# Performance work log

Measured on AMD Instinct MI355X. Metric: run time of the kernel, lower is better.

## Reference

```python
import jax, jax.numpy as jnp
import numpy as np

DIM = 1024
NUM_EXPERTS = 8
ACTIVE_EXPERTS = 2
EXPERT_DIM = 2048


def setup_inputs() -> dict:
    key = jax.random.key(0)
    k1, k2, k3, k4 = jax.random.split(key, 4)
    x = jax.random.normal(k1, (1, 2048, DIM), dtype=jnp.float32)
    gate_w = jax.random.normal(k2, (NUM_EXPERTS, DIM), dtype=jnp.float32) * 0.02
    balance_bias = jnp.zeros((NUM_EXPERTS,), dtype=jnp.float32)
    w1 = jax.random.normal(k3, (NUM_EXPERTS, EXPERT_DIM, DIM), dtype=jnp.float32) * 0.02
    w2 = jax.random.normal(k4, (NUM_EXPERTS, DIM, EXPERT_DIM), dtype=jnp.float32) * 0.02
    return {"x": x, "gate_w": gate_w, "balance_bias": balance_bias, "w1": w1, "w2": w2}


def reference(x, gate_w, balance_bias, w1, w2):
    B, S, D = x.shape
    T = B * S
    xf = x.reshape(T, D)
    # gating: sigmoid scores with load-balance bias, then top-k
    gate_logits = jnp.einsum('td,ed->te', xf, gate_w)
    gate_scores = jax.nn.sigmoid(gate_logits + balance_bias)
    topk_scores, topk_idx = jax.lax.top_k(gate_scores, ACTIVE_EXPERTS)
    topk_scores = topk_scores / (topk_scores.sum(axis=-1, keepdims=True) + 1e-6)
    # scatter normalized scores into dense combine weights [T, E]
    comb = jnp.zeros((T, NUM_EXPERTS), dtype=x.dtype)
    comb = comb.at[jnp.arange(T)[:, None], topk_idx].add(topk_scores)
    # expert FFNs (dense over experts; combine weight zeroes unselected)
    h = jax.nn.silu(jnp.einsum('td,ehd->teh', xf, w1))   # [T, E, expert_dim]
    expert_out = jnp.einsum('teh,edh->ted', h, w2)        # [T, E, D]
    out = jnp.einsum('te,ted->td', comb, expert_out)
    return out.reshape(B, S, D)
```

## Files before the change

### kernel.cpp

```cpp
#include <hip/hip_runtime.h>

#define T 2048
#define DIM 1024
#define NE 8
#define ED 2048
#define NSLOT (T * 2)
#define KSPLIT 2

#define BM 128
#define BN 64
#define BK 32

typedef __attribute__((ext_vector_type(8))) short s8v;
typedef __attribute__((ext_vector_type(4))) float f32x4;

__device__ __forceinline__ short f2bf(float f) {
    union { float f; unsigned u; } v;
    v.f = f;
    unsigned r = 0x7FFFu + ((v.u >> 16) & 1u);
    v.u += r;
    return (short)(v.u >> 16);
}

__device__ __forceinline__ float bf2f(short s) {
    union { unsigned u; float f; } v;
    v.u = ((unsigned)(unsigned short)s) << 16;
    return v.f;
}

__device__ __forceinline__ unsigned pkbf2(float lo, float hi) {
    union { float f; unsigned u; } a, b;
    a.f = lo; b.f = hi;
    return __builtin_amdgcn_perm(b.u + 0x8000u, a.u + 0x8000u, 0x07060302u);
}

__device__ __forceinline__ void glds16(const void* g, void* l) {
    __builtin_amdgcn_global_load_lds(
        (const __attribute__((address_space(1))) void*)g,
        (__attribute__((address_space(3))) void*)l, 16, 0, 0);
}

__global__ __launch_bounds__(256) void convert_kernel(const float* __restrict__ src,
                                                      short* __restrict__ dst, int n8) {
    int stride = gridDim.x * 256;
    for (int i = blockIdx.x * 256 + threadIdx.x; i < n8; i += stride) {
        float4 a = ((const float4*)src)[2 * i];
        float4 b = ((const float4*)src)[2 * i + 1];
        uint4 o = { pkbf2(a.x, a.y), pkbf2(a.z, a.w), pkbf2(b.x, b.y), pkbf2(b.z, b.w) };
        ((uint4*)dst)[i] = o;
    }
}

__global__ void router_kernel(const float* __restrict__ x,
                              const float* __restrict__ gw,
                              const float* __restrict__ bias,
                              short* __restrict__ xb,
                              int* __restrict__ counts,
                              int* __restrict__ top2i,
                              float* __restrict__ top2w) {
    int wid = threadIdx.x >> 6;
    int lane = threadIdx.x & 63;
    int t = blockIdx.x * 4 + wid;

    const float* xr = x + (size_t)t * DIM + lane * 16;
    float4 xv[4];
#pragma unroll
    for (int j = 0; j < 4; ++j) xv[j] = *(const float4*)(xr + j * 4);

    s8v o0, o1;
#pragma unroll
    for (int j = 0; j < 2; ++j) {
        o0[j * 4 + 0] = f2bf(xv[j].x); o0[j * 4 + 1] = f2bf(xv[j].y);
        o0[j * 4 + 2] = f2bf(xv[j].z); o0[j * 4 + 3] = f2bf(xv[j].w);
        o1[j * 4 + 0] = f2bf(xv[j + 2].x); o1[j * 4 + 1] = f2bf(xv[j + 2].y);
        o1[j * 4 + 2] = f2bf(xv[j + 2].z); o1[j * 4 + 3] = f2bf(xv[j + 2].w);
    }
    *(s8v*)(xb + (size_t)t * DIM + lane * 16) = o0;
    *(s8v*)(xb + (size_t)t * DIM + lane * 16 + 8) = o1;

    float sc[NE];
#pragma unroll
    for (int e = 0; e < NE; ++e) {
        const float* gr = gw + e * DIM + lane * 16;
        float p = 0.f;
#pragma unroll
        for (int j = 0; j < 4; ++j) {
            float4 g = *(const float4*)(gr + j * 4);
            p += xv[j].x * g.x + xv[j].y * g.y + xv[j].z * g.z + xv[j].w * g.w;
        }
#pragma unroll
        for (int off = 32; off; off >>= 1) p += __shfl_xor(p, off, 64);
        sc[e] = 1.f / (1.f + __expf(-(p + bias[e])));
    }
    int b0 = 0; float s0 = sc[0];
#pragma unroll
    for (int e = 1; e < NE; ++e) if (sc[e] > s0) { s0 = sc[e]; b0 = e; }
    int b1 = -1; float s1 = -1e30f;
#pragma unroll
    for (int e = 0; e < NE; ++e) if (e != b0 && sc[e] > s1) { s1 = sc[e]; b1 = e; }
    float inv = 1.f / (s0 + s1 + 1e-6f);
    if (lane == 0) {
        top2i[t * 2 + 0] = b0; top2i[t * 2 + 1] = b1;
        top2w[t * 2 + 0] = s0 * inv; top2w[t * 2 + 1] = s1 * inv;
        atomicAdd(&counts[b0], 1);
        atomicAdd(&counts[b1], 1);
    }
}

__global__ __launch_bounds__(256) void plan_kernel(
    const int* __restrict__ counts, const int* __restrict__ top2i,
    int* __restrict__ offsets, int* __restrict__ tok_list, int* __restrict__ slot_of) {
    __shared__ int soff[NE];
    __shared__ int srun[NE];
    if (threadIdx.x == 0) {
        int a = 0;
        for (int e = 0; e < NE; ++e) { soff[e] = a; offsets[e] = a; a += counts[e]; srun[e] = 0; }
    }
    __syncthreads();
    for (int t = threadIdx.x; t < T; t += 256) {
#pragma unroll
        for (int k = 0; k < 2; ++k) {
            int e = top2i[t * 2 + k];
            int pos = atomicAdd(&srun[e], 1);
            int slot = soff[e] + pos;
            tok_list[slot] = t;
            slot_of[t * 2 + k] = slot;
        }
    }
}

template <int BF>
__global__ __launch_bounds__(256) void ffn1_kernel(
    const short* __restrict__ xb, const float* __restrict__ w1,
    const short* __restrict__ wb,
    const int* __restrict__ counts, const int* __restrict__ offsets,
    const int* __restrict__ tok_list, short* __restrict__ h) {
    int e = blockIdx.x & 7;
    int j = blockIdx.x >> 3;
    int cnt = counts[e];
    const int NT = ED / BN;
    int mt = (cnt + BM - 1) / BM;
    if (j >= mt * NT) return;
    int m0 = (j / NT) * BM;
    int n0 = (j % NT) * BN;
    int off = offsets[e];

    __shared__ __align__(16) short As[2][4][BM][8];
    __shared__ __align__(16) short Bs[2][4][BN][8];

    int tid = threadIdx.x;
    int lane = tid & 63, w = tid >> 6;
    int mo = w * 32;
    int lrow = lane & 15, lq = lane >> 4;

    f32x4 acc[2][4];
#pragma unroll
    for (int mi = 0; mi < 2; ++mi)
#pragma unroll
        for (int ni = 0; ni < 4; ++ni) acc[mi][ni] = (f32x4){0.f, 0.f, 0.f, 0.f};

    int ra0 = m0 + lane;      if (ra0 > cnt - 1) ra0 = cnt - 1;
    int ra1 = m0 + 64 + lane; if (ra1 > cnt - 1) ra1 = cnt - 1;
    const short* a0 = xb + (size_t)tok_list[off + ra0] * DIM + w * 8;
    const short* a1 = xb + (size_t)tok_list[off + ra1] * DIM + w * 8;

    const short* b0 = wb + ((size_t)e * ED + n0 + lane) * DIM + w * 8;
    int br = tid >> 2, bq = tid & 3;
    const float* bp = w1 + ((size_t)e * ED + n0 + br) * DIM + bq * 8;

    const int NK = DIM / BK;

    if constexpr (BF) {
        auto stage = [&](int s, int b) {
            int k0 = s * BK;
            glds16(a0 + k0, &As[b][w][0][0]);
            glds16(a1 + k0, &As[b][w][64][0]);
            glds16(b0 + k0, &Bs[b][w][0][0]);
        };
        stage(0, 0);
        for (int kk = 0; kk < NK; ++kk) {
            int cur = kk & 1, nxt = cur ^ 1;
            __syncthreads();
            if (kk + 1 < NK) stage(kk + 1, nxt);
            s8v af[2], bfr[4];
#pragma unroll
            for (int mi = 0; mi < 2; ++mi) af[mi] = *(const s8v*)&As[cur][lq][mo + mi * 16 + lrow][0];
#pragma unroll
            for (int ni = 0; ni < 4; ++ni) bfr[ni] = *(const s8v*)&Bs[cur][lq][ni * 16 + lrow][0];
#pragma unroll
            for (int mi = 0; mi < 2; ++mi)
#pragma unroll
                for (int ni = 0; ni < 4; ++ni)
                    acc[mi][ni] = __builtin_amdgcn_mfma_f32_16x16x32_bf16(af[mi], bfr[ni], acc[mi][ni], 0, 0, 0);
        }
    } else {
        float4 L0, L1;
        glds16(a0, &As[0][w][0][0]);
        glds16(a1, &As[0][w][64][0]);
        L0 = *(const float4*)(bp); L1 = *(const float4*)(bp + 4);
        {
            uint4 p0 = { pkbf2(L0.x, L0.y), pkbf2(L0.z, L0.w), pkbf2(L1.x, L1.y), pkbf2(L1.z, L1.w) };
            *(uint4*)&Bs[0][bq][br][0] = p0;
        }
        L0 = *(const float4*)(bp + BK); L1 = *(const float4*)(bp + BK + 4);
        for (int kk = 0; kk < NK; ++kk) {
            int cur = kk & 1, nxt = cur ^ 1;
            __syncthreads();
            if (kk + 1 < NK) {
                int k0 = (kk + 1) * BK;
                glds16(a0 + k0, &As[nxt][w][0][0]);
                glds16(a1 + k0, &As[nxt][w][64][0]);
                uint4 p0 = { pkbf2(L0.x, L0.y), pkbf2(L0.z, L0.w), pkbf2(L1.x, L1.y), pkbf2(L1.z, L1.w) };
                *(uint4*)&Bs[nxt][bq][br][0] = p0;
                if (kk + 2 < NK) {
                    const float* bpp = bp + (kk + 2) * BK;
                    L0 = *(const float4*)(bpp); L1 = *(const float4*)(bpp + 4);
                }
            }
            s8v af[2], bfr[4];
#pragma unroll
            for (int mi = 0; mi < 2; ++mi) af[mi] = *(const s8v*)&As[cur][lq][mo + mi * 16 + lrow][0];
#pragma unroll
            for (int ni = 0; ni < 4; ++ni) bfr[ni] = *(const s8v*)&Bs[cur][lq][ni * 16 + lrow][0];
#pragma unroll
            for (int mi = 0; mi < 2; ++mi)
#pragma unroll
                for (int ni = 0; ni < 4; ++ni)
                    acc[mi][ni] = __builtin_amdgcn_mfma_f32_16x16x32_bf16(af[mi], bfr[ni], acc[mi][ni], 0, 0, 0);
        }
    }

#pragma unroll
    for (int mi = 0; mi < 2; ++mi) {
#pragma unroll
        for (int ni = 0; ni < 4; ++ni) {
            int ln = n0 + ni * 16 + lrow;
#pragma unroll
            for (int r = 0; r < 4; ++r) {
                int row = m0 + mo + mi * 16 + lq * 4 + r;
                if (row < cnt) {
                    float v = acc[mi][ni][r];
                    v = v / (1.f + __expf(-v));
                    h[(size_t)(off + row) * ED + ln] = f2bf(v);
                }
            }
        }
    }
}

template <int BF>
__global__ __launch_bounds__(256) void ffn2_kernel(
    const short* __restrict__ h, const float* __restrict__ w2,
    const short* __restrict__ wb,
    const int* __restrict__ counts, const int* __restrict__ offsets,
    short* __restrict__ eo) {
    int e = blockIdx.x & 7;
    int j = blockIdx.x >> 3;
    int cnt = counts[e];
    const int NT = DIM / BN;
    int mt = (cnt + BM - 1) / BM;
    if (j >= mt * NT * KSPLIT) return;
    int ksp = j & 1; j >>= 1;
    int m0 = (j / NT) * BM;
    int n0 = (j % NT) * BN;
    int off = offsets[e];
    const int kbase = ksp * (ED / KSPLIT);

    __shared__ __align__(16) short As[2][4][BM][8];
    __shared__ __align__(16) short Bs[2][4][BN][8];

    int tid = threadIdx.x;
    int lane = tid & 63, w = tid >> 6;
    int mo = w * 32;
    int lrow = lane & 15, lq = lane >> 4;

    f32x4 acc[2][4];
#pragma unroll
    for (int mi = 0; mi < 2; ++mi)
#pragma unroll
        for (int ni = 0; ni < 4; ++ni) acc[mi][ni] = (f32x4){0.f, 0.f, 0.f, 0.f};

    int ra0 = m0 + lane;      if (ra0 > cnt - 1) ra0 = cnt - 1;
    int ra1 = m0 + 64 + lane; if (ra1 > cnt - 1) ra1 = cnt - 1;
    const short* a0 = h + (size_t)(off + ra0) * ED + kbase + w * 8;
    const short* a1 = h + (size_t)(off + ra1) * ED + kbase + w * 8;

    const short* b0 = wb + ((size_t)e * DIM + n0 + lane) * ED + kbase + w * 8;
    int br = tid >> 2, bq = tid & 3;
    const float* bp = w2 + ((size_t)e * DIM + n0 + br) * ED + kbase + bq * 8;

    const int NK = (ED / KSPLIT) / BK;

    if constexpr (BF) {
        auto stage = [&](int s, int b) {
            int k0 = s * BK;
            glds16(a0 + k0, &As[b][w][0][0]);
            glds16(a1 + k0, &As[b][w][64][0]);
            glds16(b0 + k0, &Bs[b][w][0][0]);
        };
        stage(0, 0);
        for (int kk = 0; kk < NK; ++kk) {
            int cur = kk & 1, nxt = cur ^ 1;
            __syncthreads();
            if (kk + 1 < NK) stage(kk + 1, nxt);
            s8v af[2], bfr[4];
#pragma unroll
            for (int mi = 0; mi < 2; ++mi) af[mi] = *(const s8v*)&As[cur][lq][mo + mi * 16 + lrow][0];
#pragma unroll
            for (int ni = 0; ni < 4; ++ni) bfr[ni] = *(const s8v*)&Bs[cur][lq][ni * 16 + lrow][0];
#pragma unroll
            for (int mi = 0; mi < 2; ++mi)
#pragma unroll
                for (int ni = 0; ni < 4; ++ni)
                    acc[mi][ni] = __builtin_amdgcn_mfma_f32_16x16x32_bf16(af[mi], bfr[ni], acc[mi][ni], 0, 0, 0);
        }
    } else {
        float4 L0, L1;
        glds16(a0, &As[0][w][0][0]);
        glds16(a1, &As[0][w][64][0]);
        L0 = *(const float4*)(bp); L1 = *(const float4*)(bp + 4);
        {
            uint4 p0 = { pkbf2(L0.x, L0.y), pkbf2(L0.z, L0.w), pkbf2(L1.x, L1.y), pkbf2(L1.z, L1.w) };
            *(uint4*)&Bs[0][bq][br][0] = p0;
        }
        L0 = *(const float4*)(bp + BK); L1 = *(const float4*)(bp + BK + 4);
        for (int kk = 0; kk < NK; ++kk) {
            int cur = kk & 1, nxt = cur ^ 1;
            __syncthreads();
            if (kk + 1 < NK) {
                int k0 = (kk + 1) * BK;
                glds16(a0 + k0, &As[nxt][w][0][0]);
                glds16(a1 + k0, &As[nxt][w][64][0]);
                uint4 p0 = { pkbf2(L0.x, L0.y), pkbf2(L0.z, L0.w), pkbf2(L1.x, L1.y), pkbf2(L1.z, L1.w) };
                *(uint4*)&Bs[nxt][bq][br][0] = p0;
                if (kk + 2 < NK) {
                    const float* bpp = bp + (kk + 2) * BK;
                    L0 = *(const float4*)(bpp); L1 = *(const float4*)(bpp + 4);
                }
            }
            s8v af[2], bfr[4];
#pragma unroll
            for (int mi = 0; mi < 2; ++mi) af[mi] = *(const s8v*)&As[cur][lq][mo + mi * 16 + lrow][0];
#pragma unroll
            for (int ni = 0; ni < 4; ++ni) bfr[ni] = *(const s8v*)&Bs[cur][lq][ni * 16 + lrow][0];
#pragma unroll
            for (int mi = 0; mi < 2; ++mi)
#pragma unroll
                for (int ni = 0; ni < 4; ++ni)
                    acc[mi][ni] = __builtin_amdgcn_mfma_f32_16x16x32_bf16(af[mi], bfr[ni], acc[mi][ni], 0, 0, 0);
        }
    }

    short* eop = eo + (size_t)ksp * NSLOT * DIM;
#pragma unroll
    for (int mi = 0; mi < 2; ++mi) {
#pragma unroll
        for (int ni = 0; ni < 4; ++ni) {
            int ln = n0 + ni * 16 + lrow;
#pragma unroll
            for (int r = 0; r < 4; ++r) {
                int row = m0 + mo + mi * 16 + lq * 4 + r;
                if (row < cnt) {
                    eop[(size_t)(off + row) * DIM + ln] = f2bf(acc[mi][ni][r]);
                }
            }
        }
    }
}

__global__ __launch_bounds__(256) void combine_kernel(
    const short* __restrict__ eo, const int* __restrict__ slot_of,
    const float* __restrict__ top2w, float* __restrict__ out) {
    int idx = blockIdx.x * 256 + threadIdx.x;
    int t = idx >> 7;
    int c = idx & 127;
    int s0 = slot_of[2 * t], s1 = slot_of[2 * t + 1];
    float w0 = top2w[2 * t], w1 = top2w[2 * t + 1];
    const short* e0 = eo;
    const short* e1 = eo + (size_t)NSLOT * DIM;
    s8v a0 = *(const s8v*)(e0 + (size_t)s0 * DIM + c * 8);
    s8v a1 = *(const s8v*)(e1 + (size_t)s0 * DIM + c * 8);
    s8v b0 = *(const s8v*)(e0 + (size_t)s1 * DIM + c * 8);
    s8v b1 = *(const s8v*)(e1 + (size_t)s1 * DIM + c * 8);
    float4 o[2];
#pragma unroll
    for (int j = 0; j < 8; ++j) {
        float v = w0 * (bf2f(a0[j]) + bf2f(a1[j])) + w1 * (bf2f(b0[j]) + bf2f(b1[j]));
        ((float*)o)[j] = v;
    }
    float4* op = (float4*)(out + (size_t)t * DIM + c * 8);
    op[0] = o[0];
    op[1] = o[1];
}

extern "C" void kernel_launch(void* const* d_in, const int* in_sizes, int n_in,
                              void* d_out, int out_size, void* d_ws, size_t ws_size,
                              hipStream_t stream) {
    const float* x    = (const float*)d_in[0];
    const float* gw   = (const float*)d_in[1];
    const float* bias = (const float*)d_in[2];
    const float* w1   = (const float*)d_in[3];
    const float* w2   = (const float*)d_in[4];
    float* out = (float*)d_out;

    char* ws = (char*)d_ws;
    short* xb = (short*)ws;
    short* h  = (short*)(ws + (4ull << 20));
    short* eo = (short*)(ws + (20ull << 20));
    char* meta = ws + (36ull << 20);
    int*   counts   = (int*)(meta);
    int*   offsets  = (int*)(meta + 64);
    int*   tok_list = (int*)(meta + 128);
    int*   slot_of  = (int*)(meta + 128 + 4 * NSLOT);
    int*   top2i    = (int*)(meta + 128 + 8 * NSLOT);
    float* top2w    = (float*)(meta + 128 + 8 * NSLOT + 8 * T);
    short* wb       = (short*)(ws + (37ull << 20));

    bool bf = ws_size >= (70ull << 20);

    hipMemsetAsync(counts, 0, 32, stream);

    const int GRID_FFN1 = 8 * 16 * (ED / BN);
    const int GRID_FFN2 = 8 * 16 * (DIM / BN) * KSPLIT;

    if (bf) {
        convert_kernel<<<2048, 256, 0, stream>>>(w1, wb, NE * ED * DIM / 8);
    }
    router_kernel<<<T / 4, 256, 0, stream>>>(x, gw, bias, xb, counts, top2i, top2w);
    plan_kernel<<<1, 256, 0, stream>>>(counts, top2i, offsets, tok_list, slot_of);
    if (bf) {
        ffn1_kernel<1><<<GRID_FFN1, 256, 0, stream>>>(xb, w1, wb, counts, offsets, tok_list, h);
        convert_kernel<<<2048, 256, 0, stream>>>(w2, wb, NE * DIM * ED / 8);
        ffn2_kernel<1><<<GRID_FFN2, 256, 0, stream>>>(h, w2, wb, counts, offsets, eo);
    } else {
        ffn1_kernel<0><<<GRID_FFN1, 256, 0, stream>>>(xb, w1, nullptr, counts, offsets, tok_list, h);
        ffn2_kernel<0><<<GRID_FFN2, 256, 0, stream>>>(h, w2, nullptr, counts, offsets, eo);
    }
    combine_kernel<<<T * DIM / 8 / 256, 256, 0, stream>>>(eo, slot_of, top2w, out);
}
```

Before: 347.4 us.

## Pre-tile weights and gathered activations into MFMA-ready layout, drop split-K

```diff
diff --git a/kernel.cpp b/kernel.cpp
--- a/kernel.cpp
+++ b/kernel.cpp
@@ -4,8 +4,8 @@
 #define DIM 1024
 #define NE 8
 #define ED 2048
-#define NSLOT (T * 2)
-#define KSPLIT 2
+#define PSLOT 5120
+#define MT_MAX 16
 
 #define BM 128
 #define BN 64
@@ -40,21 +40,39 @@
         (__attribute__((address_space(3))) void*)l, 16, 0, 0);
 }
 
-__global__ __launch_bounds__(256) void convert_kernel(const float* __restrict__ src,
-                                                      short* __restrict__ dst, int n8) {
-    int stride = gridDim.x * 256;
-    for (int i = blockIdx.x * 256 + threadIdx.x; i < n8; i += stride) {
-        float4 a = ((const float4*)src)[2 * i];
-        float4 b = ((const float4*)src)[2 * i + 1];
-        uint4 o = { pkbf2(a.x, a.y), pkbf2(a.z, a.w), pkbf2(b.x, b.y), pkbf2(b.z, b.w) };
-        ((uint4*)dst)[i] = o;
+__global__ __launch_bounds__(256) void convert1_kernel(const float* __restrict__ w1,
+                                                       short* __restrict__ wbt) {
+    int wid = blockIdx.x * 4 + (threadIdx.x >> 6);
+    int lane = threadIdx.x & 63;
+    int e = wid >> 10, rem = wid & 1023, nb = rem >> 5, kk = rem & 31;
+    const float4* src = (const float4*)(w1 + ((size_t)(e * ED + nb * 64 + lane)) * DIM + kk * 32);
+    short* dst = wbt + ((size_t)(e * 32 + nb) * 128 + kk * 4) * 512 + lane * 8;
+#pragma unroll
+    for (int q = 0; q < 4; ++q) {
+        float4 f0 = src[2 * q], f1 = src[2 * q + 1];
+        uint4 o = { pkbf2(f0.x, f0.y), pkbf2(f0.z, f0.w), pkbf2(f1.x, f1.y), pkbf2(f1.z, f1.w) };
+        *(uint4*)(dst + q * 512) = o;
+    }
+}
+
+__global__ __launch_bounds__(256) void convert2_kernel(const float* __restrict__ w2,
+                                                       short* __restrict__ wbt) {
+    int wid = blockIdx.x * 4 + (threadIdx.x >> 6);
+    int lane = threadIdx.x & 63;
+    int e = wid >> 10, rem = wid & 1023, nb = rem >> 6, kk = rem & 63;
+    const float4* src = (const float4*)(w2 + ((size_t)(e * DIM + nb * 64 + lane)) * ED + kk * 32);
+    short* dst = wbt + ((size_t)(e * 16 + nb) * 256 + kk * 4) * 512 + lane * 8;
+#pragma unroll
+    for (int q = 0; q < 4; ++q) {
+        float4 f0 = src[2 * q], f1 = src[2 * q + 1];
+        uint4 o = { pkbf2(f0.x, f0.y), pkbf2(f0.z, f0.w), pkbf2(f1.x, f1.y), pkbf2(f1.z, f1.w) };
+        *(uint4*)(dst + q * 512) = o;
     }
 }
 
 __global__ void router_kernel(const float* __restrict__ x,
                               const float* __restrict__ gw,
                               const float* __restrict__ bias,
-                              short* __restrict__ xb,
                               int* __restrict__ counts,
                               int* __restrict__ top2i,
                               float* __restrict__ top2w) {
@@ -66,17 +84,6 @@
     float4 xv[4];
 #pragma unroll
     for (int j = 0; j < 4; ++j) xv[j] = *(const float4*)(xr + j * 4);
-
-    s8v o0, o1;
-#pragma unroll
-    for (int j = 0; j < 2; ++j) {
-        o0[j * 4 + 0] = f2bf(xv[j].x); o0[j * 4 + 1] = f2bf(xv[j].y);
-        o0[j * 4 + 2] = f2bf(xv[j].z); o0[j * 4 + 3] = f2bf(xv[j].w);
-        o1[j * 4 + 0] = f2bf(xv[j + 2].x); o1[j * 4 + 1] = f2bf(xv[j + 2].y);
-        o1[j * 4 + 2] = f2bf(xv[j + 2].z); o1[j * 4 + 3] = f2bf(xv[j + 2].w);
-    }
-    *(s8v*)(xb + (size_t)t * DIM + lane * 16) = o0;
-    *(s8v*)(xb + (size_t)t * DIM + lane * 16 + 8) = o1;
 
     float sc[NE];
 #pragma unroll
@@ -109,12 +116,16 @@
 
 __global__ __launch_bounds__(256) void plan_kernel(
     const int* __restrict__ counts, const int* __restrict__ top2i,
-    int* __restrict__ offsets, int* __restrict__ tok_list, int* __restrict__ slot_of) {
+    int* __restrict__ poff, int* __restrict__ tok_list, int* __restrict__ slot_of) {
     __shared__ int soff[NE];
     __shared__ int srun[NE];
     if (threadIdx.x == 0) {
         int a = 0;
-        for (int e = 0; e < NE; ++e) { soff[e] = a; offsets[e] = a; a += counts[e]; srun[e] = 0; }
+        for (int e = 0; e < NE; ++e) {
+            soff[e] = a; poff[e] = a;
+            a += ((counts[e] + 127) >> 7) << 7;
+            srun[e] = 0;
+        }
     }
     __syncthreads();
     for (int t = threadIdx.x; t < T; t += 256) {
@@ -127,23 +138,51 @@
             slot_of[t * 2 + k] = slot;
         }
     }
-}
-
-template <int BF>
+    __syncthreads();
+    for (int e = 0; e < NE; ++e) {
+        int cnt = counts[e];
+        int lim = ((cnt + 127) >> 7) << 7;
+        for (int i = cnt + threadIdx.x; i < lim; i += 256) tok_list[soff[e] + i] = 0;
+    }
+}
+
+__global__ __launch_bounds__(256) void gather_kernel(
+    const float* __restrict__ x, const int* __restrict__ counts,
+    const int* __restrict__ poff, const int* __restrict__ tok_list,
+    short* __restrict__ xgt) {
+    int e = blockIdx.x, mb = blockIdx.y;
+    int cnt = counts[e];
+    int mt = (cnt + 127) >> 7;
+    if (mb >= mt) return;
+    int pb = (poff[e] >> 7) + mb;
+    int r = threadIdx.x & 127, hh = threadIdx.x >> 7;
+    int tok = tok_list[poff[e] + mb * 128 + r];
+    const float4* src = (const float4*)(x + (size_t)tok * DIM + hh * 16);
+    short* dst = xgt + ((size_t)pb * 128 + hh * 2) * 1024 + r * 8;
+#pragma unroll 4
+    for (int kk = 0; kk < DIM / 32; ++kk) {
+        float4 f0 = src[0], f1 = src[1], f2 = src[2], f3 = src[3];
+        uint4 o0 = { pkbf2(f0.x, f0.y), pkbf2(f0.z, f0.w), pkbf2(f1.x, f1.y), pkbf2(f1.z, f1.w) };
+        uint4 o1 = { pkbf2(f2.x, f2.y), pkbf2(f2.z, f2.w), pkbf2(f3.x, f3.y), pkbf2(f3.z, f3.w) };
+        *(uint4*)(dst) = o0;
+        *(uint4*)(dst + 1024) = o1;
+        src += 8;
+        dst += 4 * 1024;
+    }
+}
+
 __global__ __launch_bounds__(256) void ffn1_kernel(
-    const short* __restrict__ xb, const float* __restrict__ w1,
-    const short* __restrict__ wb,
-    const int* __restrict__ counts, const int* __restrict__ offsets,
-    const int* __restrict__ tok_list, short* __restrict__ h) {
+    const short* __restrict__ xgt, const short* __restrict__ wbt,
+    const int* __restrict__ counts, const int* __restrict__ poff,
+    short* __restrict__ ht) {
     int e = blockIdx.x & 7;
     int j = blockIdx.x >> 3;
     int cnt = counts[e];
+    int mt = (cnt + 127) >> 7;
     const int NT = ED / BN;
-    int mt = (cnt + BM - 1) / BM;
     if (j >= mt * NT) return;
-    int m0 = (j / NT) * BM;
-    int n0 = (j % NT) * BN;
-    int off = offsets[e];
+    int mb = j / NT, nb = j % NT;
+    int pb = (poff[e] >> 7) + mb;
 
     __shared__ __align__(16) short As[2][4][BM][8];
     __shared__ __align__(16) short Bs[2][4][BN][8];
@@ -159,112 +198,65 @@
 #pragma unroll
         for (int ni = 0; ni < 4; ++ni) acc[mi][ni] = (f32x4){0.f, 0.f, 0.f, 0.f};
 
-    int ra0 = m0 + lane;      if (ra0 > cnt - 1) ra0 = cnt - 1;
-    int ra1 = m0 + 64 + lane; if (ra1 > cnt - 1) ra1 = cnt - 1;
-    const short* a0 = xb + (size_t)tok_list[off + ra0] * DIM + w * 8;
-    const short* a1 = xb + (size_t)tok_list[off + ra1] * DIM + w * 8;
-
-    const short* b0 = wb + ((size_t)e * ED + n0 + lane) * DIM + w * 8;
-    int br = tid >> 2, bq = tid & 3;
-    const float* bp = w1 + ((size_t)e * ED + n0 + br) * DIM + bq * 8;
-
+    const short* asrc = xgt + (size_t)pb * 128 * 1024;
+    const short* bsrc = wbt + (size_t)(e * 32 + nb) * 128 * 512;
+
+    auto stage = [&](int s, int b) {
+        int p = s * 4 + w;
+        glds16(asrc + (size_t)p * 1024 + lane * 8,       &As[b][w][0][0]);
+        glds16(asrc + (size_t)p * 1024 + 512 + lane * 8, &As[b][w][64][0]);
+        glds16(bsrc + (size_t)p * 512 + lane * 8,        &Bs[b][w][0][0]);
+    };
     const int NK = DIM / BK;
-
-    if constexpr (BF) {
-        auto stage = [&](int s, int b) {
-            int k0 = s * BK;
-            glds16(a0 + k0, &As[b][w][0][0]);
-            glds16(a1 + k0, &As[b][w][64][0]);
-            glds16(b0 + k0, &Bs[b][w][0][0]);
-        };
-        stage(0, 0);
-        for (int kk = 0; kk < NK; ++kk) {
-            int cur = kk & 1, nxt = cur ^ 1;
-            __syncthreads();
-            if (kk + 1 < NK) stage(kk + 1, nxt);
-            s8v af[2], bfr[4];
-#pragma unroll
-            for (int mi = 0; mi < 2; ++mi) af[mi] = *(const s8v*)&As[cur][lq][mo + mi * 16 + lrow][0];
-#pragma unroll
-            for (int ni = 0; ni < 4; ++ni) bfr[ni] = *(const s8v*)&Bs[cur][lq][ni * 16 + lrow][0];
-#pragma unroll
-            for (int mi = 0; mi < 2; ++mi)
-#pragma unroll
-                for (int ni = 0; ni < 4; ++ni)
-                    acc[mi][ni] = __builtin_amdgcn_mfma_f32_16x16x32_bf16(af[mi], bfr[ni], acc[mi][ni], 0, 0, 0);
-        }
-    } else {
-        float4 L0, L1;
-        glds16(a0, &As[0][w][0][0]);
-        glds16(a1, &As[0][w][64][0]);
-        L0 = *(const float4*)(bp); L1 = *(const float4*)(bp + 4);
-        {
-            uint4 p0 = { pkbf2(L0.x, L0.y), pkbf2(L0.z, L0.w), pkbf2(L1.x, L1.y), pkbf2(L1.z, L1.w) };
-            *(uint4*)&Bs[0][bq][br][0] = p0;
-        }
-        L0 = *(const float4*)(bp + BK); L1 = *(const float4*)(bp + BK + 4);
-        for (int kk = 0; kk < NK; ++kk) {
-            int cur = kk & 1, nxt = cur ^ 1;
-            __syncthreads();
-            if (kk + 1 < NK) {
-                int k0 = (kk + 1) * BK;
-                glds16(a0 + k0, &As[nxt][w][0][0]);
-                glds16(a1 + k0, &As[nxt][w][64][0]);
-                uint4 p0 = { pkbf2(L0.x, L0.y), pkbf2(L0.z, L0.w), pkbf2(L1.x, L1.y), pkbf2(L1.z, L1.w) };
-                *(uint4*)&Bs[nxt][bq][br][0] = p0;
-                if (kk + 2 < NK) {
-                    const float* bpp = bp + (kk + 2) * BK;
-                    L0 = *(const float4*)(bpp); L1 = *(const float4*)(bpp + 4);
+    stage(0, 0);
+    for (int kk = 0; kk < NK; ++kk) {
+        int cur = kk & 1, nxt = cur ^ 1;
+        __syncthreads();
+        if (kk + 1 < NK) stage(kk + 1, nxt);
+        s8v af[2], bfr[4];
+#pragma unroll
+        for (int mi = 0; mi < 2; ++mi) af[mi] = *(const s8v*)&As[cur][lq][mo + mi * 16 + lrow][0];
+#pragma unroll
+        for (int ni = 0; ni < 4; ++ni) bfr[ni] = *(const s8v*)&Bs[cur][lq][ni * 16 + lrow][0];
+#pragma unroll
+        for (int mi = 0; mi < 2; ++mi)
+#pragma unroll
+            for (int ni = 0; ni < 4; ++ni)
+                acc[mi][ni] = __builtin_amdgcn_mfma_f32_16x16x32_bf16(af[mi], bfr[ni], acc[mi][ni], 0, 0, 0);
+    }
+
+    int m0 = mb * 128;
+#pragma unroll
+    for (int mi = 0; mi < 2; ++mi) {
+#pragma unroll
+        for (int ni = 0; ni < 4; ++ni) {
+            int ln = nb * 64 + ni * 16 + lrow;
+            int koct = ln >> 3, jj = ln & 7;
+#pragma unroll
+            for (int r = 0; r < 4; ++r) {
+                int lr = mo + mi * 16 + lq * 4 + r;
+                if (m0 + lr < cnt) {
+                    float v = acc[mi][ni][r];
+                    v = v / (1.f + __expf(-v));
+                    ht[((size_t)pb * 256 + koct) * 1024 + lr * 8 + jj] = f2bf(v);
                 }
             }
-            s8v af[2], bfr[4];
-#pragma unroll
-            for (int mi = 0; mi < 2; ++mi) af[mi] = *(const s8v*)&As[cur][lq][mo + mi * 16 + lrow][0];
-#pragma unroll
-            for (int ni = 0; ni < 4; ++ni) bfr[ni] = *(const s8v*)&Bs[cur][lq][ni * 16 + lrow][0];
-#pragma unroll
-            for (int mi = 0; mi < 2; ++mi)
-#pragma unroll
-                for (int ni = 0; ni < 4; ++ni)
-                    acc[mi][ni] = __builtin_amdgcn_mfma_f32_16x16x32_bf16(af[mi], bfr[ni], acc[mi][ni], 0, 0, 0);
-        }
-    }
-
-#pragma unroll
-    for (int mi = 0; mi < 2; ++mi) {
-#pragma unroll
-        for (int ni = 0; ni < 4; ++ni) {
-            int ln = n0 + ni * 16 + lrow;
-#pragma unroll
-            for (int r = 0; r < 4; ++r) {
-                int row = m0 + mo + mi * 16 + lq * 4 + r;
-                if (row < cnt) {
-                    float v = acc[mi][ni][r];
-                    v = v / (1.f + __expf(-v));
-                    h[(size_t)(off + row) * ED + ln] = f2bf(v);
-                }
-            }
-        }
-    }
-}
-
-template <int BF>
+        }
+    }
+}
+
 __global__ __launch_bounds__(256) void ffn2_kernel(
-    const short* __restrict__ h, const float* __restrict__ w2,
-    const short* __restrict__ wb,
-    const int* __restrict__ counts, const int* __restrict__ offsets,
+    const short* __restrict__ ht, const short* __restrict__ wbt,
+    const int* __restrict__ counts, const int* __restrict__ poff,
     short* __restrict__ eo) {
     int e = blockIdx.x & 7;
     int j = blockIdx.x >> 3;
     int cnt = counts[e];
+    int mt = (cnt + 127) >> 7;
     const int NT = DIM / BN;
-    int mt = (cnt + BM - 1) / BM;
-    if (j >= mt * NT * KSPLIT) return;
-    int ksp = j & 1; j >>= 1;
-    int m0 = (j / NT) * BM;
-    int n0 = (j % NT) * BN;
-    int off = offsets[e];
-    const int kbase = ksp * (ED / KSPLIT);
+    if (j >= mt * NT) return;
+    int mb = j / NT, nb = j % NT;
+    int pb = (poff[e] >> 7) + mb;
 
     __shared__ __align__(16) short As[2][4][BM][8];
     __shared__ __align__(16) short Bs[2][4][BN][8];
@@ -280,88 +272,44 @@
 #pragma unroll
         for (int ni = 0; ni < 4; ++ni) acc[mi][ni] = (f32x4){0.f, 0.f, 0.f, 0.f};
 
-    int ra0 = m0 + lane;      if (ra0 > cnt - 1) ra0 = cnt - 1;
-    int ra1 = m0 + 64 + lane; if (ra1 > cnt - 1) ra1 = cnt - 1;
-    const short* a0 = h + (size_t)(off + ra0) * ED + kbase + w * 8;
-    const short* a1 = h + (size_t)(off + ra1) * ED + kbase + w * 8;
-
-    const short* b0 = wb + ((size_t)e * DIM + n0 + lane) * ED + kbase + w * 8;
-    int br = tid >> 2, bq = tid & 3;
-    const float* bp = w2 + ((size_t)e * DIM + n0 + br) * ED + kbase + bq * 8;
-
-    const int NK = (ED / KSPLIT) / BK;
-
-    if constexpr (BF) {
-        auto stage = [&](int s, int b) {
-            int k0 = s * BK;
-            glds16(a0 + k0, &As[b][w][0][0]);
-            glds16(a1 + k0, &As[b][w][64][0]);
-            glds16(b0 + k0, &Bs[b][w][0][0]);
-        };
-        stage(0, 0);
-        for (int kk = 0; kk < NK; ++kk) {
-            int cur = kk & 1, nxt = cur ^ 1;
-            __syncthreads();
-            if (kk + 1 < NK) stage(kk + 1, nxt);
-            s8v af[2], bfr[4];
-#pragma unroll
-            for (int mi = 0; mi < 2; ++mi) af[mi] = *(const s8v*)&As[cur][lq][mo + mi * 16 + lrow][0];
-#pragma unroll
-            for (int ni = 0; ni < 4; ++ni) bfr[ni] = *(const s8v*)&Bs[cur][lq][ni * 16 + lrow][0];
-#pragma unroll
-            for (int mi = 0; mi < 2; ++mi)
-#pragma unroll
-                for (int ni = 0; ni < 4; ++ni)
-                    acc[mi][ni] = __builtin_amdgcn_mfma_f32_16x16x32_bf16(af[mi], bfr[ni], acc[mi][ni], 0, 0, 0);
-        }
-    } else {
-        float4 L0, L1;
-        glds16(a0, &As[0][w][0][0]);
-        glds16(a1, &As[0][w][64][0]);
-        L0 = *(const float4*)(bp); L1 = *(const float4*)(bp + 4);
-        {
-            uint4 p0 = { pkbf2(L0.x, L0.y), pkbf2(L0.z, L0.w), pkbf2(L1.x, L1.y), pkbf2(L1.z, L1.w) };
-            *(uint4*)&Bs[0][bq][br][0] = p0;
-        }
-        L0 = *(const float4*)(bp + BK); L1 = *(const float4*)(bp + BK + 4);
-        for (int kk = 0; kk < NK; ++kk) {
-            int cur = kk & 1, nxt = cur ^ 1;
-            __syncthreads();
-            if (kk + 1 < NK) {
-                int k0 = (kk + 1) * BK;
-                glds16(a0 + k0, &As[nxt][w][0][0]);
-                glds16(a1 + k0, &As[nxt][w][64][0]);
-                uint4 p0 = { pkbf2(L0.x, L0.y), pkbf2(L0.z, L0.w), pkbf2(L1.x, L1.y), pkbf2(L1.z, L1.w) };
-                *(uint4*)&Bs[nxt][bq][br][0] = p0;
-                if (kk + 2 < NK) {
-                    const float* bpp = bp + (kk + 2) * BK;
-                    L0 = *(const float4*)(bpp); L1 = *(const float4*)(bpp + 4);
-                }
-            }
-            s8v af[2], bfr[4];
-#pragma unroll
-            for (int mi = 0; mi < 2; ++mi) af[mi] = *(const s8v*)&As[cur][lq][mo + mi * 16 + lrow][0];
-#pragma unroll
-            for (int ni = 0; ni < 4; ++ni) bfr[ni] = *(const s8v*)&Bs[cur][lq][ni * 16 + lrow][0];
-#pragma unroll
-            for (int mi = 0; mi < 2; ++mi)
-#pragma unroll
-                for (int ni = 0; ni < 4; ++ni)
-                    acc[mi][ni] = __builtin_amdgcn_mfma_f32_16x16x32_bf16(af[mi], bfr[ni], acc[mi][ni], 0, 0, 0);
-        }
-    }
-
-    short* eop = eo + (size_t)ksp * NSLOT * DIM;
+    const short* asrc = ht + (size_t)pb * 256 * 1024;
+    const short* bsrc = wbt + (size_t)(e * 16 + nb) * 256 * 512;
+
+    auto stage = [&](int s, int b) {
+        int p = s * 4 + w;
+        glds16(asrc + (size_t)p * 1024 + lane * 8,       &As[b][w][0][0]);
+        glds16(asrc + (size_t)p * 1024 + 512 + lane * 8, &As[b][w][64][0]);
+        glds16(bsrc + (size_t)p * 512 + lane * 8,        &Bs[b][w][0][0]);
+    };
+    const int NK = ED / BK;
+    stage(0, 0);
+    for (int kk = 0; kk < NK; ++kk) {
+        int cur = kk & 1, nxt = cur ^ 1;
+        __syncthreads();
+        if (kk + 1 < NK) stage(kk + 1, nxt);
+        s8v af[2], bfr[4];
+#pragma unroll
+        for (int mi = 0; mi < 2; ++mi) af[mi] = *(const s8v*)&As[cur][lq][mo + mi * 16 + lrow][0];
+#pragma unroll
+        for (int ni = 0; ni < 4; ++ni) bfr[ni] = *(const s8v*)&Bs[cur][lq][ni * 16 + lrow][0];
+#pragma unroll
+        for (int mi = 0; mi < 2; ++mi)
+#pragma unroll
+            for (int ni = 0; ni < 4; ++ni)
+                acc[mi][ni] = __builtin_amdgcn_mfma_f32_16x16x32_bf16(af[mi], bfr[ni], acc[mi][ni], 0, 0, 0);
+    }
+
+    int m0 = mb * 128;
 #pragma unroll
     for (int mi = 0; mi < 2; ++mi) {
 #pragma unroll
         for (int ni = 0; ni < 4; ++ni) {
-            int ln = n0 + ni * 16 + lrow;
+            int ln = nb * 64 + ni * 16 + lrow;
 #pragma unroll
             for (int r = 0; r < 4; ++r) {
-                int row = m0 + mo + mi * 16 + lq * 4 + r;
-                if (row < cnt) {
-                    eop[(size_t)(off + row) * DIM + ln] = f2bf(acc[mi][ni][r]);
+                int lr = mo + mi * 16 + lq * 4 + r;
+                if (m0 + lr < cnt) {
+                    eo[((size_t)pb * 128 + lr) * 1024 + ln] = f2bf(acc[mi][ni][r]);
                 }
             }
         }
@@ -376,16 +324,12 @@
     int c = idx & 127;
     int s0 = slot_of[2 * t], s1 = slot_of[2 * t + 1];
     float w0 = top2w[2 * t], w1 = top2w[2 * t + 1];
-    const short* e0 = eo;
-    const short* e1 = eo + (size_t)NSLOT * DIM;
-    s8v a0 = *(const s8v*)(e0 + (size_t)s0 * DIM + c * 8);
-    s8v a1 = *(const s8v*)(e1 + (size_t)s0 * DIM + c * 8);
-    s8v b0 = *(const s8v*)(e0 + (size_t)s1 * DIM + c * 8);
-    s8v b1 = *(const s8v*)(e1 + (size_t)s1 * DIM + c * 8);
+    s8v a0 = *(const s8v*)(eo + (size_t)s0 * DIM + c * 8);
+    s8v b0 = *(const s8v*)(eo + (size_t)s1 * DIM + c * 8);
     float4 o[2];
 #pragma unroll
     for (int j = 0; j < 8; ++j) {
-        float v = w0 * (bf2f(a0[j]) + bf2f(a1[j])) + w1 * (bf2f(b0[j]) + bf2f(b1[j]));
+        float v = w0 * bf2f(a0[j]) + w1 * bf2f(b0[j]);
         ((float*)o)[j] = v;
     }
     float4* op = (float4*)(out + (size_t)t * DIM + c * 8);
@@ -404,37 +348,26 @@
     float* out = (float*)d_out;
 
     char* ws = (char*)d_ws;
-    short* xb = (short*)ws;
-    short* h  = (short*)(ws + (4ull << 20));
-    short* eo = (short*)(ws + (20ull << 20));
-    char* meta = ws + (36ull << 20);
+    short* xgt = (short*)ws;
+    short* eo  = xgt;
+    short* ht  = (short*)(ws + 10485760ull);
+    char* meta = ws + 31457280ull;
     int*   counts   = (int*)(meta);
-    int*   offsets  = (int*)(meta + 64);
+    int*   poff     = (int*)(meta + 64);
     int*   tok_list = (int*)(meta + 128);
-    int*   slot_of  = (int*)(meta + 128 + 4 * NSLOT);
-    int*   top2i    = (int*)(meta + 128 + 8 * NSLOT);
-    float* top2w    = (float*)(meta + 128 + 8 * NSLOT + 8 * T);
-    short* wb       = (short*)(ws + (37ull << 20));
-
-    bool bf = ws_size >= (70ull << 20);
+    int*   slot_of  = (int*)(meta + 128 + 4 * PSLOT);
+    int*   top2i    = (int*)(meta + 128 + 4 * PSLOT + 8 * T);
+    float* top2w    = (float*)(meta + 128 + 4 * PSLOT + 16 * T);
+    short* wbt = (short*)(ws + 33554432ull);
 
     hipMemsetAsync(counts, 0, 32, stream);
 
-    const int GRID_FFN1 = 8 * 16 * (ED / BN);
-    const int GRID_FFN2 = 8 * 16 * (DIM / BN) * KSPLIT;
-
-    if (bf) {
-        convert_kernel<<<2048, 256, 0, stream>>>(w1, wb, NE * ED * DIM / 8);
-    }
-    router_kernel<<<T / 4, 256, 0, stream>>>(x, gw, bias, xb, counts, top2i, top2w);
-    plan_kernel<<<1, 256, 0, stream>>>(counts, top2i, offsets, tok_list, slot_of);
-    if (bf) {
-        ffn1_kernel<1><<<GRID_FFN1, 256, 0, stream>>>(xb, w1, wb, counts, offsets, tok_list, h);
-        convert_kernel<<<2048, 256, 0, stream>>>(w2, wb, NE * DIM * ED / 8);
-        ffn2_kernel<1><<<GRID_FFN2, 256, 0, stream>>>(h, w2, wb, counts, offsets, eo);
-    } else {
-        ffn1_kernel<0><<<GRID_FFN1, 256, 0, stream>>>(xb, w1, nullptr, counts, offsets, tok_list, h);
-        ffn2_kernel<0><<<GRID_FFN2, 256, 0, stream>>>(h, w2, nullptr, counts, offsets, eo);
-    }
+    convert1_kernel<<<2048, 256, 0, stream>>>(w1, wbt);
+    router_kernel<<<T / 4, 256, 0, stream>>>(x, gw, bias, counts, top2i, top2w);
+    plan_kernel<<<1, 256, 0, stream>>>(counts, top2i, poff, tok_list, slot_of);
+    gather_kernel<<<dim3(NE, MT_MAX), 256, 0, stream>>>(x, counts, poff, tok_list, xgt);
+    ffn1_kernel<<<NE * MT_MAX * (ED / BN), 256, 0, stream>>>(xgt, wbt, counts, poff, ht);
+    convert2_kernel<<<2048, 256, 0, stream>>>(w2, wbt);
+    ffn2_kernel<<<NE * MT_MAX * (DIM / BN), 256, 0, stream>>>(ht, wbt, counts, poff, eo);
     combine_kernel<<<T * DIM / 8 / 256, 256, 0, stream>>>(eo, slot_of, top2w, out);
 }
```

After: 345.1 us. Within noise of the previous version (-0.7%).
